# Kernel optimization log

Hardware: AMD Instinct MI355X
Metric: run time of the kernel (lower is better)

Reference implementation:

```python
import jax, jax.numpy as jnp
import numpy as np

B, T, EMB = 2, 2048, 1024
H, D = 16, 64          # num_heads, head_dim; hidden = H*D = 1024
SCALE = D ** (-0.5)


def setup_inputs() -> dict:
    key = jax.random.key(0)
    k1, k2, k3, k4, k5 = jax.random.split(key, 5)
    return {
        "x":    jax.random.normal(k1, (B, T, EMB), dtype=jnp.float32),
        "Wqkv": jax.random.normal(k2, (EMB, 3 * H * D), dtype=jnp.float32) * (EMB ** -0.5),
        "bqkv": jax.random.normal(k3, (3 * H * D,), dtype=jnp.float32) * 0.02,
        "Wout": jax.random.normal(k4, (H * D, EMB), dtype=jnp.float32) * ((H * D) ** -0.5),
        "bout": jax.random.normal(k5, (EMB,), dtype=jnp.float32) * 0.02,
    }


def reference(x, Wqkv, bqkv, Wout, bout):
    b, t, _ = x.shape
    qkv = x @ Wqkv + bqkv                                   # [b, t, 3*H*D]
    q, k, v = jnp.split(qkv, 3, axis=-1)
    split_heads = lambda a: a.reshape(b, t, H, D).transpose(0, 2, 1, 3)  # [b,h,t,d]
    q, k, v = split_heads(q), split_heads(k), split_heads(v)

    scores = jnp.einsum('bhid,bhjd->bhij', q, k) * SCALE    # [b,h,t,t]
    causal = jnp.tril(jnp.ones((t, t), dtype=bool))         # lower-triangular mask
    scores = jnp.where(causal, scores, -jnp.inf)
    attn = jax.nn.softmax(scores, axis=-1)                  # dropout: eval mode (identity)

    out = jnp.einsum('bhij,bhjd->bhid', attn, v)            # [b,h,t,d]
    out = out.transpose(0, 2, 1, 3).reshape(b, t, H * D)    # [b,t,H*D]
    return out @ Wout + bout                                # [b,t,EMB]
```

## Files before the change

kernel.cpp:

```cpp
#include <hip/hip_runtime.h>
#include <hip/hip_bf16.h>
#include <stdint.h>

#define B_ 2
#define T_ 2048
#define EMB_ 1024
#define H_ 16
#define D_ 64
#define QS_ 0.1803368801111f

typedef __attribute__((ext_vector_type(8))) __bf16 bf8_t;
typedef __attribute__((ext_vector_type(8))) short s8_t;
typedef __attribute__((ext_vector_type(4))) short s4_t;
typedef __attribute__((ext_vector_type(4))) float f4_t;
typedef __attribute__((ext_vector_type(2))) unsigned int u32x2;

#if __has_builtin(__builtin_amdgcn_exp2f)
#define EXP2(x) __builtin_amdgcn_exp2f(x)
#else
#define EXP2(x) exp2f(x)
#endif

__device__ __forceinline__ short f2b(float f) {
    union { float f; uint32_t u; } c; c.f = f;
    uint32_t r = (c.u + 0x7FFFu + ((c.u >> 16) & 1u)) >> 16;
    return (short)(uint16_t)r;
}

__device__ __forceinline__ uint32_t cvtpk(float lo, float hi) {
    uint32_t r;
    asm volatile("v_cvt_pk_bf16_f32 %0, %1, %2" : "=v"(r) : "v"(lo), "v"(hi));
    return r;
}

__device__ __forceinline__ void glds16(const void* g, void* l) {
    __builtin_amdgcn_global_load_lds(
        (const __attribute__((address_space(1))) unsigned int*)g,
        (__attribute__((address_space(3))) unsigned int*)l, 16, 0, 0);
}

__global__ __launch_bounds__(256)
void cast_f32_bf16(const float* __restrict__ in, short* __restrict__ outp) {
    const size_t i = ((size_t)blockIdx.x * 256 + threadIdx.x) * 4;
    f4_t v = *(const f4_t*)(in + i);
    s4_t r; r[0] = f2b(v[0]); r[1] = f2b(v[1]); r[2] = f2b(v[2]); r[3] = f2b(v[3]);
    *(s4_t*)(outp + i) = r;
}

__global__ __launch_bounds__(256)
void transpose_f2b(const float* __restrict__ in, short* __restrict__ outp,
                   int K, int N, int nscale, float sc) {
    __shared__ short Ts[64][72];
    const int t = threadIdx.x;
    const int r = t >> 4, c = (t & 15) * 4;
    const int n0 = blockIdx.x * 64, k0 = blockIdx.y * 64;
    #pragma unroll
    for (int it = 0; it < 4; it++) {
        const int rr = it * 16 + r;
        f4_t v = *(const f4_t*)(in + (size_t)(k0 + rr) * N + n0 + c);
        #pragma unroll
        for (int j = 0; j < 4; j++) {
            const float s = (n0 + c + j < nscale) ? sc : 1.0f;
            Ts[c + j][rr] = f2b(v[j] * s);
        }
    }
    __syncthreads();
    #pragma unroll
    for (int it = 0; it < 4; it++) {
        const int rr = it * 16 + r;
        s4_t o;
        #pragma unroll
        for (int j = 0; j < 4; j++) o[j] = Ts[rr][c + j];
        *(s4_t*)(outp + (size_t)(n0 + rr) * K + k0 + c) = o;
    }
}

__global__ __launch_bounds__(256)
void transpose_v(const short* __restrict__ qkv, short* __restrict__ vt) {
    __shared__ short Ts[64][72];
    const int t = threadIdx.x;
    const int r = t >> 4, c = (t & 15) * 4;
    const int bh = blockIdx.y, bb = bh >> 4, hh = bh & 15;
    const int t0 = blockIdx.x * 64;
    #pragma unroll
    for (int it = 0; it < 4; it++) {
        const int rr = it * 16 + r;
        s4_t v = *(const s4_t*)(qkv + (size_t)(bb * T_ + t0 + rr) * 3072 + 2048 + hh * 64 + c);
        #pragma unroll
        for (int j = 0; j < 4; j++) Ts[c + j][rr] = v[j];
    }
    __syncthreads();
    #pragma unroll
    for (int it = 0; it < 4; it++) {
        const int rr = it * 16 + r;
        s4_t o;
        #pragma unroll
        for (int j = 0; j < 4; j++) o[j] = Ts[rr][c + j];
        *(s4_t*)(vt + (size_t)(bh * 64 + rr) * T_ + t0 + c) = o;
    }
}

__global__ __launch_bounds__(256)
void gemm_bt(const short* __restrict__ A, const short* __restrict__ Bt,
             const float* __restrict__ bias, short* __restrict__ Cb,
             float* __restrict__ Cf, int M, int N, int K, int outf32, int qsflag)
{
    __shared__ __align__(16) short As[128 * 64];
    __shared__ __align__(16) short Bs[128 * 64];

    const int t = threadIdx.x;
    const int L = t & 63, l16 = L & 15, quad = L >> 4;
    const int w = t >> 6, wm = w >> 1, wn = w & 1;
    const int n0 = blockIdx.x * 128, m0 = blockIdx.y * 128;

    f4_t acc[4][4];
    #pragma unroll
    for (int i = 0; i < 4; i++)
        #pragma unroll
        for (int j = 0; j < 4; j++) acc[i][j] = (f4_t){0.f, 0.f, 0.f, 0.f};

    for (int k0 = 0; k0 < K; k0 += 64) {
        __syncthreads();
        #pragma unroll
        for (int it = 0; it < 4; it++) {
            const int c = it * 256 + t;
            const int row = c >> 3, pc = c & 7;
            const int cc = pc ^ (row & 7);
            glds16(A + (size_t)(m0 + row) * K + k0 + cc * 8, &As[c * 8]);
            glds16(Bt + (size_t)(n0 + row) * K + k0 + cc * 8, &Bs[c * 8]);
        }
        asm volatile("s_waitcnt vmcnt(0)" ::: "memory");
        __syncthreads();

        #pragma unroll
        for (int kc = 0; kc < 2; kc++) {
            bf8_t a[4], b[4];
            #pragma unroll
            for (int i = 0; i < 4; i++) {
                const int row = wm * 64 + i * 16 + l16;
                const int ch = (kc * 4 + quad) ^ (row & 7);
                a[i] = *(const bf8_t*)(&As[row * 64 + ch * 8]);
            }
            #pragma unroll
            for (int j = 0; j < 4; j++) {
                const int row = wn * 64 + j * 16 + l16;
                const int ch = (kc * 4 + quad) ^ (row & 7);
                b[j] = *(const bf8_t*)(&Bs[row * 64 + ch * 8]);
            }
            #pragma unroll
            for (int i = 0; i < 4; i++)
                #pragma unroll
                for (int j = 0; j < 4; j++)
                    acc[i][j] = __builtin_amdgcn_mfma_f32_16x16x32_bf16(a[i], b[j], acc[i][j], 0, 0, 0);
        }
    }

    #pragma unroll
    for (int j = 0; j < 4; j++) {
        const int n = n0 + wn * 64 + j * 16 + l16;
        float bv = bias[n];
        if (qsflag && n < 1024) bv *= QS_;
        #pragma unroll
        for (int i = 0; i < 4; i++) {
            #pragma unroll
            for (int r = 0; r < 4; r++) {
                const int m = m0 + wm * 64 + i * 16 + quad * 4 + r;
                const float val = acc[i][j][r] + bv;
                if (outf32) Cf[(size_t)m * N + n] = val;
                else        Cb[(size_t)m * N + n] = f2b(val);
            }
        }
    }
}

__global__ __launch_bounds__(256)
void gemm_bt_n64(const short* __restrict__ A, const short* __restrict__ Bt,
                 const float* __restrict__ bias, float* __restrict__ Cf,
                 int M, int N, int K)
{
    __shared__ __align__(16) short As[2][128 * 64];
    __shared__ __align__(16) short Bs[2][64 * 64];

    const int t = threadIdx.x;
    const int L = t & 63, l16 = L & 15, quad = L >> 4;
    const int w = t >> 6;
    const int n0 = blockIdx.x * 64, m0 = blockIdx.y * 128;

    f4_t acc[2][4];
    #pragma unroll
    for (int i = 0; i < 2; i++)
        #pragma unroll
        for (int j = 0; j < 4; j++) acc[i][j] = (f4_t){0.f, 0.f, 0.f, 0.f};

#define GSTAGE(kt_, buf_)                                                      \
    {                                                                          \
        const int k0_ = (kt_) * 64;                                            \
        _Pragma("unroll")                                                      \
        for (int it = 0; it < 4; it++) {                                       \
            const int c = it * 256 + t;                                        \
            const int row = c >> 3, pc = c & 7;                                \
            const int cc = pc ^ (row & 7);                                     \
            glds16(A + (size_t)(m0 + row) * K + k0_ + cc * 8, &As[buf_][c * 8]); \
        }                                                                      \
        _Pragma("unroll")                                                      \
        for (int it = 0; it < 2; it++) {                                       \
            const int c = it * 256 + t;                                        \
            const int row = c >> 3, pc = c & 7;                                \
            const int cc = pc ^ (row & 7);                                     \
            glds16(Bt + (size_t)(n0 + row) * K + k0_ + cc * 8, &Bs[buf_][c * 8]); \
        }                                                                      \
    }

    const int nkt = K >> 6;
    GSTAGE(0, 0);
    for (int kt = 0; kt < nkt; kt++) {
        const int cur = kt & 1;
        if (kt + 1 < nkt) {
            GSTAGE(kt + 1, cur ^ 1);
            asm volatile("s_waitcnt vmcnt(6)" ::: "memory");
        } else {
            asm volatile("s_waitcnt vmcnt(0)" ::: "memory");
        }
        __builtin_amdgcn_s_barrier();

        #pragma unroll
        for (int kc = 0; kc < 2; kc++) {
            bf8_t a[2], b[4];
            #pragma unroll
            for (int i = 0; i < 2; i++) {
                const int row = w * 32 + i * 16 + l16;
                const int ch = (kc * 4 + quad) ^ (row & 7);
                a[i] = *(const bf8_t*)(&As[cur][row * 64 + ch * 8]);
            }
            #pragma unroll
            for (int j = 0; j < 4; j++) {
                const int row = j * 16 + l16;
                const int ch = (kc * 4 + quad) ^ (row & 7);
                b[j] = *(const bf8_t*)(&Bs[cur][row * 64 + ch * 8]);
            }
            #pragma unroll
            for (int i = 0; i < 2; i++)
                #pragma unroll
                for (int j = 0; j < 4; j++)
                    acc[i][j] = __builtin_amdgcn_mfma_f32_16x16x32_bf16(a[i], b[j], acc[i][j], 0, 0, 0);
        }
        __builtin_amdgcn_s_barrier();
    }
#undef GSTAGE

    #pragma unroll
    for (int j = 0; j < 4; j++) {
        const int n = n0 + j * 16 + l16;
        const float bv = bias[n];
        #pragma unroll
        for (int i = 0; i < 2; i++) {
            #pragma unroll
            for (int r = 0; r < 4; r++) {
                const int m = m0 + w * 32 + i * 16 + quad * 4 + r;
                Cf[(size_t)m * N + n] = acc[i][j][r] + bv;
            }
        }
    }
}

__global__ __launch_bounds__(256)
void attn_kernel(const short* __restrict__ qkv, const short* __restrict__ vt,
                 short* __restrict__ ab)
{
    __shared__ __align__(16) short Ks[2][64 * 64];
    __shared__ __align__(16) short Vs[2][64 * 64];
    __shared__ __align__(16) short Ps[4][16 * 64];

    const int t = threadIdx.x;
    const int L = t & 63, l16 = L & 15, quad = L >> 4;
    const int w = t >> 6;

    const int qi = 31 - (blockIdx.x >> 5);
    const int bh = blockIdx.x & 31;
    const int bb = bh >> 4, hh = bh & 15;
    const int qb = qi * 64;
    const int wrow = qb + w * 16;
    const int qrow = wrow + l16;

    const size_t qoff = (size_t)(bb * T_ + wrow + l16) * 3072 + hh * 64;
    const bf8_t qa0 = *(const bf8_t*)(qkv + qoff + quad * 8);
    const bf8_t qa1 = *(const bf8_t*)(qkv + qoff + 32 + quad * 8);

    s8_t os_;
    #pragma unroll
    for (int i = 0; i < 8; i++) os_[i] = (short)0x3F80;
    const bf8_t ones = *(const bf8_t*)&os_;

    f4_t lacc = {0.f, 0.f, 0.f, 0.f};
    f4_t o_acc[4];
    #pragma unroll
    for (int nc = 0; nc < 4; nc++) o_acc[nc] = (f4_t){0.f, 0.f, 0.f, 0.f};

#define STAGE(ktile, buf)                                                      \
    {                                                                          \
        const int ktb_ = (ktile) * 64;                                         \
        _Pragma("unroll")                                                      \
        for (int it = 0; it < 2; it++) {                                       \
            const int c = it * 256 + t;                                        \
            const int row = c >> 3, pc = c & 7;                                \
            const int cc = pc ^ (row & 7);                                     \
            glds16(qkv + (size_t)(bb * T_ + ktb_ + row) * 3072 + 1024 + hh * 64 + cc * 8, \
                   &Ks[buf][c * 8]);                                           \
            glds16(vt + (size_t)(bh * 64 + row) * T_ + ktb_ + cc * 8,          \
                   &Vs[buf][c * 8]);                                           \
        }                                                                      \
    }

    const int nkt = qi + 1;
    STAGE(0, 0);
    for (int kt = 0; kt < nkt; kt++) {
        const int cur = kt & 1;
        if (kt + 1 < nkt) {
            STAGE(kt + 1, cur ^ 1);
            asm volatile("s_waitcnt vmcnt(4)" ::: "memory");
        } else {
            asm volatile("s_waitcnt vmcnt(0)" ::: "memory");
        }
        __builtin_amdgcn_s_barrier();

        if (kt * 64 <= wrow + 15) {
            const int ktb = kt * 64;
            const bool domask = (ktb + 63 > wrow);

            f4_t s[4];
            #pragma unroll
            for (int nh = 0; nh < 4; nh++) {
                const int key = nh * 16 + l16;
                const int ch0 = quad ^ (key & 7);
                const int ch1 = (4 + quad) ^ (key & 7);
                bf8_t k0f = *(const bf8_t*)(&Ks[cur][key * 64 + ch0 * 8]);
                bf8_t k1f = *(const bf8_t*)(&Ks[cur][key * 64 + ch1 * 8]);
                f4_t z = {0.f, 0.f, 0.f, 0.f};
                z = __builtin_amdgcn_mfma_f32_16x16x32_bf16(k0f, qa0, z, 0, 0, 0);
                z = __builtin_amdgcn_mfma_f32_16x16x32_bf16(k1f, qa1, z, 0, 0, 0);
                s[nh] = z;
            }

            char* const psb = (char*)&Ps[w][0];
            #pragma unroll
            for (int nh = 0; nh < 4; nh++) {
                float v0 = s[nh][0], v1 = s[nh][1], v2 = s[nh][2], v3 = s[nh][3];
                if (domask) {
                    const int keyb = ktb + nh * 16 + quad * 4;
                    if (keyb     > qrow) v0 = -1e30f;
                    if (keyb + 1 > qrow) v1 = -1e30f;
                    if (keyb + 2 > qrow) v2 = -1e30f;
                    if (keyb + 3 > qrow) v3 = -1e30f;
                }
                u32x2 pk2;
                pk2.x = cvtpk(EXP2(v0), EXP2(v1));
                pk2.y = cvtpk(EXP2(v2), EXP2(v3));
                *(u32x2*)(psb + l16 * 128 + ((nh * 32 + quad * 8) ^ ((l16 & 7) << 4))) = pk2;
            }
            asm volatile("s_waitcnt lgkmcnt(0)" ::: "memory");

            const bf8_t pa0 = *(const bf8_t*)(psb + l16 * 128 + ((quad * 16) ^ ((l16 & 7) << 4)));
            const bf8_t pa1 = *(const bf8_t*)(psb + l16 * 128 + ((64 + quad * 16) ^ ((l16 & 7) << 4)));

            lacc = __builtin_amdgcn_mfma_f32_16x16x32_bf16(pa0, ones, lacc, 0, 0, 0);
            lacc = __builtin_amdgcn_mfma_f32_16x16x32_bf16(pa1, ones, lacc, 0, 0, 0);

            #pragma unroll
            for (int nc = 0; nc < 4; nc++) {
                const int d = nc * 16 + l16;
                const int ch0 = quad ^ (d & 7);
                const int ch1 = (4 + quad) ^ (d & 7);
                bf8_t v0f = *(const bf8_t*)(&Vs[cur][d * 64 + ch0 * 8]);
                bf8_t v1f = *(const bf8_t*)(&Vs[cur][d * 64 + ch1 * 8]);
                o_acc[nc] = __builtin_amdgcn_mfma_f32_16x16x32_bf16(pa0, v0f, o_acc[nc], 0, 0, 0);
                o_acc[nc] = __builtin_amdgcn_mfma_f32_16x16x32_bf16(pa1, v1f, o_acc[nc], 0, 0, 0);
            }
        }
        __builtin_amdgcn_s_barrier();
    }
#undef STAGE

    #pragma unroll
    for (int r = 0; r < 4; r++) {
        const float rl = __builtin_amdgcn_rcpf(lacc[r]);
        const int row = wrow + quad * 4 + r;
        #pragma unroll
        for (int nc = 0; nc < 4; nc++) {
            ab[(size_t)(bb * T_ + row) * 1024 + hh * 64 + nc * 16 + l16] =
                f2b(o_acc[nc][r] * rl);
        }
    }
}

extern "C" void kernel_launch(void* const* d_in, const int* in_sizes, int n_in,
                              void* d_out, int out_size, void* d_ws, size_t ws_size,
                              hipStream_t stream) {
    const float* x    = (const float*)d_in[0];
    const float* Wqkv = (const float*)d_in[1];
    const float* bqkv = (const float*)d_in[2];
    const float* Wout = (const float*)d_in[3];
    const float* bout = (const float*)d_in[4];
    float* out = (float*)d_out;

    short* ws   = (short*)d_ws;
    short* xb   = ws;
    short* wqt  = xb + (size_t)4096 * 1024;
    short* qkvt = wqt + (size_t)3072 * 1024;
    short* vt   = (short*)d_out;
    short* ab   = xb;

    cast_f32_bf16<<<4096, 256, 0, stream>>>(x, xb);
    transpose_f2b<<<dim3(48, 16), 256, 0, stream>>>(Wqkv, wqt, 1024, 3072, 1024, QS_);

    gemm_bt<<<dim3(24, 32), 256, 0, stream>>>(xb, wqt, bqkv, qkvt, nullptr,
                                              4096, 3072, 1024, 0, 1);

    transpose_v<<<dim3(32, 32), 256, 0, stream>>>(qkvt, vt);
    transpose_f2b<<<dim3(16, 16), 256, 0, stream>>>(Wout, wqt, 1024, 1024, 0, 1.0f);

    attn_kernel<<<1024, 256, 0, stream>>>(qkvt, vt, ab);

    gemm_bt_n64<<<dim3(16, 32), 256, 0, stream>>>(ab, wqt, bout, out,
                                                  4096, 1024, 1024);
}
```

Before: 183.1 us.

## Load V fragments directly from global into registers instead of LDS staging

Removes the shared-memory staging of the transposed V tile. Each wave now loads its V MFMA operands straight from global memory into registers at the top of every key tile, with vmcnt waits retuned to match. The per-wave causal skip check is dropped, and s_setprio is raised around the MFMA sections. This saves LDS space and LDS read traffic, but each of the four waves redundantly loads the same V data from global/L2 and depends on global latency being hidden.

```diff
diff --git a/kernel.cpp b/kernel.cpp
--- a/kernel.cpp
+++ b/kernel.cpp
@@ -268,7 +268,6 @@
                  short* __restrict__ ab)
 {
     __shared__ __align__(16) short Ks[2][64 * 64];
-    __shared__ __align__(16) short Vs[2][64 * 64];
     __shared__ __align__(16) short Ps[4][16 * 64];
 
     const int t = threadIdx.x;
@@ -286,6 +285,8 @@
     const bf8_t qa0 = *(const bf8_t*)(qkv + qoff + quad * 8);
     const bf8_t qa1 = *(const bf8_t*)(qkv + qoff + 32 + quad * 8);
 
+    const short* vbase = vt + (size_t)(bh * 64 + l16) * T_ + quad * 8;
+
     s8_t os_;
     #pragma unroll
     for (int i = 0; i < 8; i++) os_[i] = (short)0x3F80;
@@ -296,7 +297,7 @@
     #pragma unroll
     for (int nc = 0; nc < 4; nc++) o_acc[nc] = (f4_t){0.f, 0.f, 0.f, 0.f};
 
-#define STAGE(ktile, buf)                                                      \
+#define STAGE_K(ktile, buf)                                                    \
     {                                                                          \
         const int ktb_ = (ktile) * 64;                                         \
         _Pragma("unroll")                                                      \
@@ -306,79 +307,89 @@
             const int cc = pc ^ (row & 7);                                     \
             glds16(qkv + (size_t)(bb * T_ + ktb_ + row) * 3072 + 1024 + hh * 64 + cc * 8, \
                    &Ks[buf][c * 8]);                                           \
-            glds16(vt + (size_t)(bh * 64 + row) * T_ + ktb_ + cc * 8,          \
-                   &Vs[buf][c * 8]);                                           \
         }                                                                      \
     }
 
     const int nkt = qi + 1;
-    STAGE(0, 0);
+    STAGE_K(0, 0);
     for (int kt = 0; kt < nkt; kt++) {
         const int cur = kt & 1;
+        const int ktb = kt * 64;
+
+        bf8_t vA[4], vB[4];
+        #pragma unroll
+        for (int nc = 0; nc < 4; nc++) {
+            vA[nc] = *(const bf8_t*)(vbase + (size_t)nc * 16 * T_ + ktb);
+            vB[nc] = *(const bf8_t*)(vbase + (size_t)nc * 16 * T_ + ktb + 32);
+        }
+
         if (kt + 1 < nkt) {
-            STAGE(kt + 1, cur ^ 1);
-            asm volatile("s_waitcnt vmcnt(4)" ::: "memory");
+            STAGE_K(kt + 1, cur ^ 1);
+            asm volatile("s_waitcnt vmcnt(10)" ::: "memory");
+        } else {
+            asm volatile("s_waitcnt vmcnt(8)" ::: "memory");
+        }
+        __builtin_amdgcn_s_barrier();
+
+        const bool domask = (ktb + 63 > wrow);
+
+        f4_t s[4];
+        __builtin_amdgcn_s_setprio(1);
+        #pragma unroll
+        for (int nh = 0; nh < 4; nh++) {
+            const int key = nh * 16 + l16;
+            const int ch0 = quad ^ (key & 7);
+            const int ch1 = (4 + quad) ^ (key & 7);
+            bf8_t k0f = *(const bf8_t*)(&Ks[cur][key * 64 + ch0 * 8]);
+            bf8_t k1f = *(const bf8_t*)(&Ks[cur][key * 64 + ch1 * 8]);
+            f4_t z = {0.f, 0.f, 0.f, 0.f};
+            z = __builtin_amdgcn_mfma_f32_16x16x32_bf16(k0f, qa0, z, 0, 0, 0);
+            z = __builtin_amdgcn_mfma_f32_16x16x32_bf16(k1f, qa1, z, 0, 0, 0);
+            s[nh] = z;
+        }
+        __builtin_amdgcn_s_setprio(0);
+
+        char* const psb = (char*)&Ps[w][0];
+        #pragma unroll
+        for (int nh = 0; nh < 4; nh++) {
+            float v0 = s[nh][0], v1 = s[nh][1], v2 = s[nh][2], v3 = s[nh][3];
+            if (domask) {
+                const int keyb = ktb + nh * 16 + quad * 4;
+                if (keyb     > qrow) v0 = -1e30f;
+                if (keyb + 1 > qrow) v1 = -1e30f;
+                if (keyb + 2 > qrow) v2 = -1e30f;
+                if (keyb + 3 > qrow) v3 = -1e30f;
+            }
+            u32x2 pk2;
+            pk2.x = cvtpk(EXP2(v0), EXP2(v1));
+            pk2.y = cvtpk(EXP2(v2), EXP2(v3));
+            *(u32x2*)(psb + l16 * 128 + ((nh * 32 + quad * 8) ^ ((l16 & 7) << 4))) = pk2;
+        }
+        asm volatile("s_waitcnt lgkmcnt(0)" ::: "memory");
+
+        const bf8_t pa0 = *(const bf8_t*)(psb + l16 * 128 + ((quad * 16) ^ ((l16 & 7) << 4)));
+        const bf8_t pa1 = *(const bf8_t*)(psb + l16 * 128 + ((64 + quad * 16) ^ ((l16 & 7) << 4)));
+
+        if (kt + 1 < nkt) {
+            asm volatile("s_waitcnt vmcnt(2)" ::: "memory");
         } else {
             asm volatile("s_waitcnt vmcnt(0)" ::: "memory");
         }
+
+        __builtin_amdgcn_s_setprio(1);
+        lacc = __builtin_amdgcn_mfma_f32_16x16x32_bf16(pa0, ones, lacc, 0, 0, 0);
+        lacc = __builtin_amdgcn_mfma_f32_16x16x32_bf16(pa1, ones, lacc, 0, 0, 0);
+
+        #pragma unroll
+        for (int nc = 0; nc < 4; nc++) {
+            o_acc[nc] = __builtin_amdgcn_mfma_f32_16x16x32_bf16(pa0, vA[nc], o_acc[nc], 0, 0, 0);
+            o_acc[nc] = __builtin_amdgcn_mfma_f32_16x16x32_bf16(pa1, vB[nc], o_acc[nc], 0, 0, 0);
+        }
+        __builtin_amdgcn_s_setprio(0);
+
         __builtin_amdgcn_s_barrier();
-
-        if (kt * 64 <= wrow + 15) {
-            const int ktb = kt * 64;
-            const bool domask = (ktb + 63 > wrow);
-
-            f4_t s[4];
-            #pragma unroll
-            for (int nh = 0; nh < 4; nh++) {
-                const int key = nh * 16 + l16;
-                const int ch0 = quad ^ (key & 7);
-                const int ch1 = (4 + quad) ^ (key & 7);
-                bf8_t k0f = *(const bf8_t*)(&Ks[cur][key * 64 + ch0 * 8]);
-                bf8_t k1f = *(const bf8_t*)(&Ks[cur][key * 64 + ch1 * 8]);
-                f4_t z = {0.f, 0.f, 0.f, 0.f};
-                z = __builtin_amdgcn_mfma_f32_16x16x32_bf16(k0f, qa0, z, 0, 0, 0);
-                z = __builtin_amdgcn_mfma_f32_16x16x32_bf16(k1f, qa1, z, 0, 0, 0);
-                s[nh] = z;
-            }
-
-            char* const psb = (char*)&Ps[w][0];
-            #pragma unroll
-            for (int nh = 0; nh < 4; nh++) {
-                float v0 = s[nh][0], v1 = s[nh][1], v2 = s[nh][2], v3 = s[nh][3];
-                if (domask) {
-                    const int keyb = ktb + nh * 16 + quad * 4;
-                    if (keyb     > qrow) v0 = -1e30f;
-                    if (keyb + 1 > qrow) v1 = -1e30f;
-                    if (keyb + 2 > qrow) v2 = -1e30f;
-                    if (keyb + 3 > qrow) v3 = -1e30f;
-                }
-                u32x2 pk2;
-                pk2.x = cvtpk(EXP2(v0), EXP2(v1));
-                pk2.y = cvtpk(EXP2(v2), EXP2(v3));
-                *(u32x2*)(psb + l16 * 128 + ((nh * 32 + quad * 8) ^ ((l16 & 7) << 4))) = pk2;
-            }
-            asm volatile("s_waitcnt lgkmcnt(0)" ::: "memory");
-
-            const bf8_t pa0 = *(const bf8_t*)(psb + l16 * 128 + ((quad * 16) ^ ((l16 & 7) << 4)));
-            const bf8_t pa1 = *(const bf8_t*)(psb + l16 * 128 + ((64 + quad * 16) ^ ((l16 & 7) << 4)));
-
-            lacc = __builtin_amdgcn_mfma_f32_16x16x32_bf16(pa0, ones, lacc, 0, 0, 0);
-            lacc = __builtin_amdgcn_mfma_f32_16x16x32_bf16(pa1, ones, lacc, 0, 0, 0);
-
-            #pragma unroll
-            for (int nc = 0; nc < 4; nc++) {
-                const int d = nc * 16 + l16;
-                const int ch0 = quad ^ (d & 7);
-                const int ch1 = (4 + quad) ^ (d & 7);
-                bf8_t v0f = *(const bf8_t*)(&Vs[cur][d * 64 + ch0 * 8]);
-                bf8_t v1f = *(const bf8_t*)(&Vs[cur][d * 64 + ch1 * 8]);
-                o_acc[nc] = __builtin_amdgcn_mfma_f32_16x16x32_bf16(pa0, v0f, o_acc[nc], 0, 0, 0);
-                o_acc[nc] = __builtin_amdgcn_mfma_f32_16x16x32_bf16(pa1, v1f, o_acc[nc], 0, 0, 0);
-            }
-        }
-        __builtin_amdgcn_s_barrier();
-    }
-#undef STAGE
+    }
+#undef STAGE_K
 
     #pragma unroll
     for (int r = 0; r < 4; r++) {
```

Result: slower. 229.0 us (+25.1%).
